# Kernel tuning notes

Hardware: AMD Instinct MI355X
Metric: run time of the kernel (lower is better)

## Reference

```python
import jax, jax.numpy as jnp
import numpy as np

B, LQ, LK = 4, 256, 512
DQ, DK, DV = 512, 512, 512
H = 256
NEG = -1e6


def setup_inputs() -> dict:
    key = jax.random.key(0)
    ks = jax.random.split(key, 7)
    queries = jax.random.normal(ks[0], (B, LQ, DQ), dtype=jnp.float32)
    keys = jax.random.normal(ks[1], (B, LK, DK), dtype=jnp.float32)
    values = jax.random.normal(ks[2], (B, LK, DV), dtype=jnp.float32)
    valid_lens = jax.random.randint(ks[3], (B,), 1, LK + 1).astype(jnp.int32)
    # learned params (Linear without bias): store as (in, out) so x @ W matches torch x @ W.T
    Wq = jax.random.normal(ks[4], (DQ, H), dtype=jnp.float32) * (1.0 / np.sqrt(DQ))
    Wk = jax.random.normal(ks[5], (DK, H), dtype=jnp.float32) * (1.0 / np.sqrt(DK))
    wv = jax.random.normal(ks[6], (H,), dtype=jnp.float32) * (1.0 / np.sqrt(H))
    return {"queries": queries, "keys": keys, "values": values,
            "valid_lens": valid_lens, "Wq": Wq, "Wk": Wk, "wv": wv}


def reference(queries, keys, values, valid_lens, Wq, Wk, wv):
    q = jnp.einsum('bqd,dh->bqh', queries, Wq)          # (B,Lq,H)
    k = jnp.einsum('bkd,dh->bkh', keys, Wk)             # (B,Lk,H)
    feats = jnp.tanh(q[:, :, None, :] + k[:, None, :, :])  # (B,Lq,Lk,H)
    scores = jnp.einsum('bqkh,h->bqk', feats, wv)        # (B,Lq,Lk)
    mask = jnp.arange(LK)[None, None, :] < valid_lens[:, None, None]  # (B,1,Lk)
    attn = jax.nn.softmax(jnp.where(mask, scores, NEG), axis=-1)
    return jnp.einsum('bqk,bkv->bqv', attn, values)      # (B,Lq,Dv)
```

## Files before the change

kernel.cpp:

```cpp
#include <hip/hip_runtime.h>

#define B_   4
#define LQ_  256
#define LK_  512
#define DIN_ 512
#define H_   256
#define DV_  512

#define L2E 1.4426950408889634f

__global__ __launch_bounds__(256) void proj_partial_kernel(
    const float* __restrict__ Q, const float* __restrict__ K,
    const float* __restrict__ Wq, const float* __restrict__ Wk,
    const int* __restrict__ valid_lens,
    float* __restrict__ qpart, float* __restrict__ ekTpart) {
  __shared__ float xs[64][68];
  __shared__ float ws[64][132];

  const int blk = blockIdx.x;
  const bool isQ = blk < 128;
  int b, row0, h0, ds;
  if (isQ) {
    ds = blk & 3; h0 = ((blk >> 2) & 1) * 128;
    const int rt = blk >> 3;
    b = rt >> 2; row0 = (rt & 3) * 64;
  } else {
    const int u = blk - 128;
    ds = u & 7; h0 = ((u >> 3) & 1) * 128;
    const int rt = u >> 4;
    b = rt & 3; row0 = (rt >> 2) * 64;
    if (row0 >= valid_lens[b]) return;
  }
  const int L = isQ ? LQ_ : LK_;
  const int dspan = isQ ? 128 : 64;
  const float* __restrict__ X  = (isQ ? Q : K) + ((size_t)(b * L + row0)) * DIN_ + ds * dspan;
  const float* __restrict__ Wb = (isQ ? Wq : Wk) + (size_t)(ds * dspan) * H_ + h0;

  const int t = threadIdx.x;
  const int hthr = t & 31;
  const int rthr = t >> 5;

  float acc[8][4];
#pragma unroll
  for (int r = 0; r < 8; ++r)
#pragma unroll
    for (int c = 0; c < 4; ++c) acc[r][c] = 0.f;

  for (int dd = 0; dd < dspan; dd += 64) {
    __syncthreads();
#pragma unroll
    for (int u = 0; u < 4; ++u) {
      const int f = t + 256 * u;
      const int r = f >> 4, c4 = (f & 15) << 2;
      *(float4*)&xs[r][c4] = *(const float4*)&X[(size_t)r * DIN_ + dd + c4];
    }
#pragma unroll
    for (int u = 0; u < 8; ++u) {
      const int f = t + 256 * u;
      const int k = f >> 5, c4 = (f & 31) << 2;
      *(float4*)&ws[k][c4] = *(const float4*)&Wb[(size_t)(dd + k) * H_ + c4];
    }
    __syncthreads();

    for (int k = 0; k < 64; k += 8) {
      float4 w4[8];
#pragma unroll
      for (int k8 = 0; k8 < 8; ++k8)
        w4[k8] = *(const float4*)&ws[k + k8][4 * hthr];
#pragma unroll
      for (int rr = 0; rr < 8; ++rr) {
        const float4 xa = *(const float4*)&xs[rthr * 8 + rr][k];
        const float4 xb = *(const float4*)&xs[rthr * 8 + rr][k + 4];
        const float xv[8] = {xa.x, xa.y, xa.z, xa.w, xb.x, xb.y, xb.z, xb.w};
#pragma unroll
        for (int k8 = 0; k8 < 8; ++k8) {
          acc[rr][0] = fmaf(xv[k8], w4[k8].x, acc[rr][0]);
          acc[rr][1] = fmaf(xv[k8], w4[k8].y, acc[rr][1]);
          acc[rr][2] = fmaf(xv[k8], w4[k8].z, acc[rr][2]);
          acc[rr][3] = fmaf(xv[k8], w4[k8].w, acc[rr][3]);
        }
      }
    }
  }

  if (isQ) {
    float* dst = qpart + (size_t)ds * (B_ * LQ_ * H_);
#pragma unroll
    for (int rr = 0; rr < 8; ++rr) {
      const int row = row0 + rthr * 8 + rr;
      float4 o = {acc[rr][0], acc[rr][1], acc[rr][2], acc[rr][3]};
      *(float4*)&dst[(size_t)(b * LQ_ + row) * H_ + h0 + 4 * hthr] = o;
    }
  } else {
    float* dst = ekTpart + (size_t)ds * (B_ * H_ * LK_);
#pragma unroll
    for (int c = 0; c < 4; ++c) {
      const int h = h0 + 4 * hthr + c;
      float* p = &dst[((size_t)b * H_ + h) * LK_ + row0 + rthr * 8];
      float4 lo = {acc[0][c], acc[1][c], acc[2][c], acc[3][c]};
      float4 hi = {acc[4][c], acc[5][c], acc[6][c], acc[7][c]};
      *(float4*)p = lo;
      *(float4*)(p + 4) = hi;
    }
  }
}

__global__ __launch_bounds__(512) void combine_ek_kernel(
    const float* __restrict__ ekTpart, float* __restrict__ ek) {
  const int k4 = blockIdx.x * 512 + threadIdx.x;
  const size_t KN4 = (size_t)B_ * H_ * LK_ / 4;
  const float4* src = (const float4*)ekTpart;
  float4 s = src[k4];
#pragma unroll
  for (int p = 1; p < 8; ++p) {
    const float4 v = src[p * KN4 + k4];
    s.x += v.x; s.y += v.y; s.z += v.z; s.w += v.w;
  }
  float4 o;
  o.x = exp2f(fminf(fmaxf(s.x * L2E, -126.f), 126.f));
  o.y = exp2f(fminf(fmaxf(s.y * L2E, -126.f), 126.f));
  o.z = exp2f(fminf(fmaxf(s.z * L2E, -126.f), 126.f));
  o.w = exp2f(fminf(fmaxf(s.w * L2E, -126.f), 126.f));
  ((float4*)ek)[k4] = o;
}

__global__ __launch_bounds__(512) void fused_attn_kernel(
    const float* __restrict__ qpart, const float* __restrict__ ek,
    const float* __restrict__ wv, const int* __restrict__ valid_lens,
    const float* __restrict__ V, float* __restrict__ out) {
  __shared__ float eqs[4][260];
  __shared__ float wvs[256];
  __shared__ float ph[2][4][512];
  __shared__ float4 p4s[LK_];
  __shared__ float redm[8][4], reds[8][4];
  __shared__ float wsum_s;

  const int blk = blockIdx.x;
  const int b  = blk & 3;
  const int i0 = (blk >> 2) * 4;
  const int vl = valid_lens[b];
  const int t = threadIdx.x;
  const int lane = t & 63, wave = t >> 6;

  const size_t QN = (size_t)B_ * LQ_ * H_;
#pragma unroll
  for (int e = t; e < 4 * H_; e += 512) {
    const int i = e >> 8, h = e & 255;
    const size_t base = (size_t)(b * LQ_ + i0 + i) * H_ + h;
    const float v = qpart[base] + qpart[QN + base] +
                    qpart[2 * QN + base] + qpart[3 * QN + base];
    eqs[i][h] = exp2f(fminf(fmaxf(v * L2E, -126.f), 126.f));
  }
  if (t < 256) wvs[t] = wv[t];
  if (t < 64) {
    float s = wv[t] + wv[t + 64] + wv[t + 128] + wv[t + 192];
#pragma unroll
    for (int off = 32; off; off >>= 1) s += __shfl_xor(s, off);
    if (t == 0) wsum_s = s;
  }
  __syncthreads();
  const float Wsum = wsum_s;

  const int jj = t & 255;
  const int ht = t >> 8;
  const int hb = ht * 128;
  const float* __restrict__ ekb = ek + (size_t)b * H_ * LK_;
  float aA[4] = {0.f, 0.f, 0.f, 0.f};
  float aB[4] = {0.f, 0.f, 0.f, 0.f};
  if (vl > 256) {
    for (int hh = 0; hh < 128; hh += 4) {
      const int h = hb + hh;
      float eA[4], eB[4];
#pragma unroll
      for (int u = 0; u < 4; ++u) {
        eA[u] = ekb[(size_t)(h + u) * LK_ + jj];
        eB[u] = ekb[(size_t)(h + u) * LK_ + jj + 256];
      }
      const float4 w4 = *(const float4*)&wvs[h];
      const float ww[4] = {w4.x, w4.y, w4.z, w4.w};
#pragma unroll
      for (int i = 0; i < 4; ++i) {
        const float4 q4 = *(const float4*)&eqs[i][h];
        const float qq[4] = {q4.x, q4.y, q4.z, q4.w};
#pragma unroll
        for (int u = 0; u < 4; ++u) {
          float p = qq[u] * eA[u];
          aA[i] = fmaf(ww[u], __builtin_amdgcn_rcpf(fmaf(p, p, 1.f)), aA[i]);
          p = qq[u] * eB[u];
          aB[i] = fmaf(ww[u], __builtin_amdgcn_rcpf(fmaf(p, p, 1.f)), aB[i]);
        }
      }
    }
  } else {
    for (int hh = 0; hh < 128; hh += 8) {
      const int h = hb + hh;
      float eA[8];
#pragma unroll
      for (int u = 0; u < 8; ++u)
        eA[u] = ekb[(size_t)(h + u) * LK_ + jj];
      const float4 wa = *(const float4*)&wvs[h];
      const float4 wb = *(const float4*)&wvs[h + 4];
      const float ww[8] = {wa.x, wa.y, wa.z, wa.w, wb.x, wb.y, wb.z, wb.w};
#pragma unroll
      for (int i = 0; i < 4; ++i) {
        const float4 qa = *(const float4*)&eqs[i][h];
        const float4 qb = *(const float4*)&eqs[i][h + 4];
        const float qq[8] = {qa.x, qa.y, qa.z, qa.w, qb.x, qb.y, qb.z, qb.w};
#pragma unroll
        for (int u = 0; u < 8; ++u) {
          float p = qq[u] * eA[u];
          aA[i] = fmaf(ww[u], __builtin_amdgcn_rcpf(fmaf(p, p, 1.f)), aA[i]);
        }
      }
    }
  }
#pragma unroll
  for (int i = 0; i < 4; ++i) {
    ph[ht][i][jj]       = aA[i];
    ph[ht][i][jj + 256] = aB[i];
  }
  __syncthreads();

  const bool valid = t < vl;
  float s[4], m[4];
#pragma unroll
  for (int i = 0; i < 4; ++i) {
    s[i] = valid ? fmaf(-2.f, ph[0][i][t] + ph[1][i][t], Wsum) : -3.0e38f;
    m[i] = s[i];
  }
#pragma unroll
  for (int off = 32; off; off >>= 1)
#pragma unroll
    for (int i = 0; i < 4; ++i) m[i] = fmaxf(m[i], __shfl_xor(m[i], off));
  if (lane == 0)
#pragma unroll
    for (int i = 0; i < 4; ++i) redm[wave][i] = m[i];
  __syncthreads();
  float e[4], sum[4];
#pragma unroll
  for (int i = 0; i < 4; ++i) {
    float mx = redm[0][i];
#pragma unroll
    for (int w = 1; w < 8; ++w) mx = fmaxf(mx, redm[w][i]);
    e[i] = valid ? __expf(s[i] - mx) : 0.f;
    sum[i] = e[i];
  }
#pragma unroll
  for (int off = 32; off; off >>= 1)
#pragma unroll
    for (int i = 0; i < 4; ++i) sum[i] += __shfl_xor(sum[i], off);
  if (lane == 0)
#pragma unroll
    for (int i = 0; i < 4; ++i) reds[wave][i] = sum[i];
  __syncthreads();
  {
    float4 pv;
    float tot[4];
#pragma unroll
    for (int i = 0; i < 4; ++i) {
      tot[i] = reds[0][i];
#pragma unroll
      for (int w = 1; w < 8; ++w) tot[i] += reds[w][i];
    }
    pv.x = e[0] * __builtin_amdgcn_rcpf(tot[0]);
    pv.y = e[1] * __builtin_amdgcn_rcpf(tot[1]);
    pv.z = e[2] * __builtin_amdgcn_rcpf(tot[2]);
    pv.w = e[3] * __builtin_amdgcn_rcpf(tot[3]);
    p4s[t] = pv;
  }
  __syncthreads();

  const float* __restrict__ Vb = V + (size_t)b * LK_ * DV_ + t;
  float a[4] = {0.f, 0.f, 0.f, 0.f};
  int j = 0;
  const int jv = vl & ~7;
  for (; j < jv; j += 8) {
    float v[8];
#pragma unroll
    for (int u = 0; u < 8; ++u) v[u] = Vb[(size_t)(j + u) * DV_];
#pragma unroll
    for (int u = 0; u < 8; ++u) {
      const float4 pp = p4s[j + u];
      a[0] = fmaf(pp.x, v[u], a[0]); a[1] = fmaf(pp.y, v[u], a[1]);
      a[2] = fmaf(pp.z, v[u], a[2]); a[3] = fmaf(pp.w, v[u], a[3]);
    }
  }
  for (; j < vl; ++j) {
    const float v = Vb[(size_t)j * DV_];
    const float4 pp = p4s[j];
    a[0] = fmaf(pp.x, v, a[0]); a[1] = fmaf(pp.y, v, a[1]);
    a[2] = fmaf(pp.z, v, a[2]); a[3] = fmaf(pp.w, v, a[3]);
  }
#pragma unroll
  for (int i = 0; i < 4; ++i)
    out[(size_t)(b * LQ_ + i0 + i) * DV_ + t] = a[i];
}

extern "C" void kernel_launch(void* const* d_in, const int* in_sizes, int n_in,
                              void* d_out, int out_size, void* d_ws, size_t ws_size,
                              hipStream_t stream) {
  const float* queries    = (const float*)d_in[0];
  const float* keys       = (const float*)d_in[1];
  const float* values     = (const float*)d_in[2];
  const int*   valid_lens = (const int*)d_in[3];
  const float* Wq         = (const float*)d_in[4];
  const float* Wk         = (const float*)d_in[5];
  const float* wv         = (const float*)d_in[6];
  float* out = (float*)d_out;

  char* ws = (char*)d_ws;
  float* qpart   = (float*)ws;
  float* ekTpart = (float*)(ws + (size_t)( 4 << 20));
  float* ek      = (float*)(ws + (size_t)(20 << 20));

  proj_partial_kernel<<<640, 256, 0, stream>>>(
      queries, keys, Wq, Wk, valid_lens, qpart, ekTpart);
  combine_ek_kernel<<<256, 512, 0, stream>>>(ekTpart, ek);
  fused_attn_kernel<<<B_ * (LQ_ / 4), 512, 0, stream>>>(
      qpart, ek, wv, valid_lens, values, out);
}
```

Measured before the change: 59.20 us.

## Precompute exp(2x) factors, halve queries per block, skip masked keys in tanh loop

New measurement: 52.47 us. -11.4%, faster.

```diff
diff --git a/kernel.cpp b/kernel.cpp
--- a/kernel.cpp
+++ b/kernel.cpp
@@ -106,7 +106,7 @@
 }
 
 __global__ __launch_bounds__(512) void combine_ek_kernel(
-    const float* __restrict__ ekTpart, float* __restrict__ ek) {
+    const float* __restrict__ ekTpart, float* __restrict__ ek2) {
   const int k4 = blockIdx.x * 512 + threadIdx.x;
   const size_t KN4 = (size_t)B_ * H_ * LK_ / 4;
   const float4* src = (const float4*)ekTpart;
@@ -117,39 +117,37 @@
     s.x += v.x; s.y += v.y; s.z += v.z; s.w += v.w;
   }
   float4 o;
-  o.x = exp2f(fminf(fmaxf(s.x * L2E, -126.f), 126.f));
-  o.y = exp2f(fminf(fmaxf(s.y * L2E, -126.f), 126.f));
-  o.z = exp2f(fminf(fmaxf(s.z * L2E, -126.f), 126.f));
-  o.w = exp2f(fminf(fmaxf(s.w * L2E, -126.f), 126.f));
-  ((float4*)ek)[k4] = o;
+  o.x = exp2f(fminf(fmaxf(s.x * (2.f * L2E), -126.f), 126.f));
+  o.y = exp2f(fminf(fmaxf(s.y * (2.f * L2E), -126.f), 126.f));
+  o.z = exp2f(fminf(fmaxf(s.z * (2.f * L2E), -126.f), 126.f));
+  o.w = exp2f(fminf(fmaxf(s.w * (2.f * L2E), -126.f), 126.f));
+  ((float4*)ek2)[k4] = o;
 }
 
 __global__ __launch_bounds__(512) void fused_attn_kernel(
-    const float* __restrict__ qpart, const float* __restrict__ ek,
+    const float* __restrict__ qpart, const float* __restrict__ ek2,
     const float* __restrict__ wv, const int* __restrict__ valid_lens,
     const float* __restrict__ V, float* __restrict__ out) {
-  __shared__ float eqs[4][260];
+  __shared__ float eqs[2][260];
   __shared__ float wvs[256];
-  __shared__ float ph[2][4][512];
-  __shared__ float4 p4s[LK_];
-  __shared__ float redm[8][4], reds[8][4];
+  __shared__ float2 p2s[LK_];
+  __shared__ float redm[8][2], reds[8][2];
   __shared__ float wsum_s;
 
   const int blk = blockIdx.x;
-  const int b  = blk & 3;
-  const int i0 = (blk >> 2) * 4;
+  const int b  = (blk & 3) ^ ((blk >> 8) & 1);
+  const int i0 = (blk >> 2) * 2;
   const int vl = valid_lens[b];
   const int t = threadIdx.x;
   const int lane = t & 63, wave = t >> 6;
 
   const size_t QN = (size_t)B_ * LQ_ * H_;
-#pragma unroll
-  for (int e = t; e < 4 * H_; e += 512) {
-    const int i = e >> 8, h = e & 255;
+  {
+    const int i = t >> 8, h = t & 255;
     const size_t base = (size_t)(b * LQ_ + i0 + i) * H_ + h;
     const float v = qpart[base] + qpart[QN + base] +
                     qpart[2 * QN + base] + qpart[3 * QN + base];
-    eqs[i][h] = exp2f(fminf(fmaxf(v * L2E, -126.f), 126.f));
+    eqs[i][h] = exp2f(fminf(fmaxf(v * (2.f * L2E), -126.f), 126.f));
   }
   if (t < 256) wvs[t] = wv[t];
   if (t < 64) {
@@ -161,84 +159,47 @@
   __syncthreads();
   const float Wsum = wsum_s;
 
-  const int jj = t & 255;
-  const int ht = t >> 8;
-  const int hb = ht * 128;
-  const float* __restrict__ ekb = ek + (size_t)b * H_ * LK_;
-  float aA[4] = {0.f, 0.f, 0.f, 0.f};
-  float aB[4] = {0.f, 0.f, 0.f, 0.f};
-  if (vl > 256) {
-    for (int hh = 0; hh < 128; hh += 4) {
-      const int h = hb + hh;
-      float eA[4], eB[4];
-#pragma unroll
-      for (int u = 0; u < 4; ++u) {
-        eA[u] = ekb[(size_t)(h + u) * LK_ + jj];
-        eB[u] = ekb[(size_t)(h + u) * LK_ + jj + 256];
-      }
-      const float4 w4 = *(const float4*)&wvs[h];
-      const float ww[4] = {w4.x, w4.y, w4.z, w4.w};
-#pragma unroll
-      for (int i = 0; i < 4; ++i) {
-        const float4 q4 = *(const float4*)&eqs[i][h];
-        const float qq[4] = {q4.x, q4.y, q4.z, q4.w};
-#pragma unroll
-        for (int u = 0; u < 4; ++u) {
-          float p = qq[u] * eA[u];
-          aA[i] = fmaf(ww[u], __builtin_amdgcn_rcpf(fmaf(p, p, 1.f)), aA[i]);
-          p = qq[u] * eB[u];
-          aB[i] = fmaf(ww[u], __builtin_amdgcn_rcpf(fmaf(p, p, 1.f)), aB[i]);
-        }
-      }
-    }
-  } else {
-    for (int hh = 0; hh < 128; hh += 8) {
-      const int h = hb + hh;
-      float eA[8];
+  const bool valid = t < vl;
+  float s[2] = {-3.0e38f, -3.0e38f};
+  if (valid) {
+    const float* __restrict__ kb = ek2 + (size_t)b * H_ * LK_ + t;
+    float a0 = 0.f, a1 = 0.f;
+    for (int h = 0; h < H_; h += 8) {
+      float kv[8];
 #pragma unroll
       for (int u = 0; u < 8; ++u)
-        eA[u] = ekb[(size_t)(h + u) * LK_ + jj];
+        kv[u] = kb[(size_t)(h + u) * LK_];
       const float4 wa = *(const float4*)&wvs[h];
       const float4 wb = *(const float4*)&wvs[h + 4];
       const float ww[8] = {wa.x, wa.y, wa.z, wa.w, wb.x, wb.y, wb.z, wb.w};
-#pragma unroll
-      for (int i = 0; i < 4; ++i) {
-        const float4 qa = *(const float4*)&eqs[i][h];
-        const float4 qb = *(const float4*)&eqs[i][h + 4];
-        const float qq[8] = {qa.x, qa.y, qa.z, qa.w, qb.x, qb.y, qb.z, qb.w};
-#pragma unroll
-        for (int u = 0; u < 8; ++u) {
-          float p = qq[u] * eA[u];
-          aA[i] = fmaf(ww[u], __builtin_amdgcn_rcpf(fmaf(p, p, 1.f)), aA[i]);
-        }
+      const float4 q0a = *(const float4*)&eqs[0][h];
+      const float4 q0b = *(const float4*)&eqs[0][h + 4];
+      const float4 q1a = *(const float4*)&eqs[1][h];
+      const float4 q1b = *(const float4*)&eqs[1][h + 4];
+      const float q0[8] = {q0a.x, q0a.y, q0a.z, q0a.w, q0b.x, q0b.y, q0b.z, q0b.w};
+      const float q1[8] = {q1a.x, q1a.y, q1a.z, q1a.w, q1b.x, q1b.y, q1b.z, q1b.w};
+#pragma unroll
+      for (int u = 0; u < 8; ++u) {
+        a0 = fmaf(ww[u], __builtin_amdgcn_rcpf(fmaf(q0[u], kv[u], 1.f)), a0);
+        a1 = fmaf(ww[u], __builtin_amdgcn_rcpf(fmaf(q1[u], kv[u], 1.f)), a1);
       }
     }
-  }
-#pragma unroll
-  for (int i = 0; i < 4; ++i) {
-    ph[ht][i][jj]       = aA[i];
-    ph[ht][i][jj + 256] = aB[i];
-  }
-  __syncthreads();
-
-  const bool valid = t < vl;
-  float s[4], m[4];
-#pragma unroll
-  for (int i = 0; i < 4; ++i) {
-    s[i] = valid ? fmaf(-2.f, ph[0][i][t] + ph[1][i][t], Wsum) : -3.0e38f;
-    m[i] = s[i];
-  }
+    s[0] = fmaf(-2.f, a0, Wsum);
+    s[1] = fmaf(-2.f, a1, Wsum);
+  }
+
+  float m[2] = {s[0], s[1]};
 #pragma unroll
   for (int off = 32; off; off >>= 1)
 #pragma unroll
-    for (int i = 0; i < 4; ++i) m[i] = fmaxf(m[i], __shfl_xor(m[i], off));
+    for (int i = 0; i < 2; ++i) m[i] = fmaxf(m[i], __shfl_xor(m[i], off));
   if (lane == 0)
 #pragma unroll
-    for (int i = 0; i < 4; ++i) redm[wave][i] = m[i];
-  __syncthreads();
-  float e[4], sum[4];
-#pragma unroll
-  for (int i = 0; i < 4; ++i) {
+    for (int i = 0; i < 2; ++i) redm[wave][i] = m[i];
+  __syncthreads();
+  float e[2], sum[2];
+#pragma unroll
+  for (int i = 0; i < 2; ++i) {
     float mx = redm[0][i];
 #pragma unroll
     for (int w = 1; w < 8; ++w) mx = fmaxf(mx, redm[w][i]);
@@ -248,30 +209,28 @@
 #pragma unroll
   for (int off = 32; off; off >>= 1)
 #pragma unroll
-    for (int i = 0; i < 4; ++i) sum[i] += __shfl_xor(sum[i], off);
+    for (int i = 0; i < 2; ++i) sum[i] += __shfl_xor(sum[i], off);
   if (lane == 0)
 #pragma unroll
-    for (int i = 0; i < 4; ++i) reds[wave][i] = sum[i];
+    for (int i = 0; i < 2; ++i) reds[wave][i] = sum[i];
   __syncthreads();
   {
-    float4 pv;
-    float tot[4];
-#pragma unroll
-    for (int i = 0; i < 4; ++i) {
+    float tot[2];
+#pragma unroll
+    for (int i = 0; i < 2; ++i) {
       tot[i] = reds[0][i];
 #pragma unroll
       for (int w = 1; w < 8; ++w) tot[i] += reds[w][i];
     }
+    float2 pv;
     pv.x = e[0] * __builtin_amdgcn_rcpf(tot[0]);
     pv.y = e[1] * __builtin_amdgcn_rcpf(tot[1]);
-    pv.z = e[2] * __builtin_amdgcn_rcpf(tot[2]);
-    pv.w = e[3] * __builtin_amdgcn_rcpf(tot[3]);
-    p4s[t] = pv;
+    p2s[t] = pv;
   }
   __syncthreads();
 
   const float* __restrict__ Vb = V + (size_t)b * LK_ * DV_ + t;
-  float a[4] = {0.f, 0.f, 0.f, 0.f};
+  float a0 = 0.f, a1 = 0.f;
   int j = 0;
   const int jv = vl & ~7;
   for (; j < jv; j += 8) {
@@ -280,20 +239,19 @@
     for (int u = 0; u < 8; ++u) v[u] = Vb[(size_t)(j + u) * DV_];
 #pragma unroll
     for (int u = 0; u < 8; ++u) {
-      const float4 pp = p4s[j + u];
-      a[0] = fmaf(pp.x, v[u], a[0]); a[1] = fmaf(pp.y, v[u], a[1]);
-      a[2] = fmaf(pp.z, v[u], a[2]); a[3] = fmaf(pp.w, v[u], a[3]);
+      const float2 pp = p2s[j + u];
+      a0 = fmaf(pp.x, v[u], a0);
+      a1 = fmaf(pp.y, v[u], a1);
     }
   }
   for (; j < vl; ++j) {
     const float v = Vb[(size_t)j * DV_];
-    const float4 pp = p4s[j];
-    a[0] = fmaf(pp.x, v, a[0]); a[1] = fmaf(pp.y, v, a[1]);
-    a[2] = fmaf(pp.z, v, a[2]); a[3] = fmaf(pp.w, v, a[3]);
-  }
-#pragma unroll
-  for (int i = 0; i < 4; ++i)
-    out[(size_t)(b * LQ_ + i0 + i) * DV_ + t] = a[i];
+    const float2 pp = p2s[j];
+    a0 = fmaf(pp.x, v, a0);
+    a1 = fmaf(pp.y, v, a1);
+  }
+  out[(size_t)(b * LQ_ + i0) * DV_ + t]     = a0;
+  out[(size_t)(b * LQ_ + i0 + 1) * DV_ + t] = a1;
 }
 
 extern "C" void kernel_launch(void* const* d_in, const int* in_sizes, int n_in,
@@ -311,11 +269,11 @@
   char* ws = (char*)d_ws;
   float* qpart   = (float*)ws;
   float* ekTpart = (float*)(ws + (size_t)( 4 << 20));
-  float* ek      = (float*)(ws + (size_t)(20 << 20));
+  float* ek2     = (float*)(ws + (size_t)(20 << 20));
 
   proj_partial_kernel<<<640, 256, 0, stream>>>(
       queries, keys, Wq, Wk, valid_lens, qpart, ekTpart);
-  combine_ek_kernel<<<256, 512, 0, stream>>>(ekTpart, ek);
-  fused_attn_kernel<<<B_ * (LQ_ / 4), 512, 0, stream>>>(
-      qpart, ek, wv, valid_lens, values, out);
-}
+  combine_ek_kernel<<<256, 512, 0, stream>>>(ekTpart, ek2);
+  fused_attn_kernel<<<512, 512, 0, stream>>>(
+      qpart, ek2, wv, valid_lens, values, out);
+}
```
